# Optimization experiments

Measured on AMD Instinct MI355X. Metric: run time of the kernel, lower is better.

Reference implementation:

```python
import jax, jax.numpy as jnp
import numpy as np

B, N = 16, 4096
D_IN, D_OUT, HID, E = 128, 128, 256, 8
SG_HID = 16  # SharedGate hidden fixed at 16 in __init__


def setup_inputs() -> dict:
    key = jax.random.key(0)
    ks = jax.random.split(key, 6)
    s = 0.05
    return {
        "x": jax.random.normal(ks[0], (B, N, D_IN), dtype=jnp.float32),
        "active_experts": jnp.ones((B, E), dtype=jnp.int32),
        # SharedGate: fc1 [16, D_IN], fc2 [D_IN, 16] (torch Linear weight is [out, in])
        "sg_w1": jax.random.normal(ks[1], (SG_HID, D_IN), dtype=jnp.float32) * s,
        "sg_w2": jax.random.normal(ks[2], (D_IN, SG_HID), dtype=jnp.float32) * s,
        # TaskSpecificGate: E linears [1, D_IN] -> stacked [E, D_IN]
        "gate_w": jax.random.normal(ks[3], (E, D_IN), dtype=jnp.float32) * s,
        # Expert MLPs (no bias): fc1 [E, HID, D_IN], fc2 [E, D_OUT, HID]
        "exp_w1": jax.random.normal(ks[4], (E, HID, D_IN), dtype=jnp.float32) * s,
        "exp_w2": jax.random.normal(ks[5], (E, D_OUT, HID), dtype=jnp.float32) * s,
    }


def reference(x, active_experts, sg_w1, sg_w2, gate_w, exp_w1, exp_w2):
    b, n, d_in = x.shape
    xf = x.reshape(-1, d_in)  # [T, D_IN], T = B*N (node-level routing)

    # SharedGate with residual: fc2(relu(fc1(x))) + x
    shared = jnp.maximum(xf @ sg_w1.T, 0.0) @ sg_w2.T + xf  # [T, D_IN]

    # Task-specific gate: per-expert scalar scores, masked softmax over experts
    scores = (shared @ gate_w.T).reshape(b, n, -1)  # [B, N, E]
    mask = active_experts.astype(bool)[:, None, :]  # [B, 1, E]
    masked = jnp.where(mask, scores, -jnp.inf)
    weights = jax.nn.softmax(masked, axis=-1)  # [B, N, E]

    # All experts (dense): batched two-layer MLP per expert
    h = jnp.maximum(jnp.einsum("td,ehd->teh", xf, exp_w1), 0.0)  # [T, E, HID]
    out = jnp.einsum("teh,eoh->teo", h, exp_w2)  # [T, E, D_OUT]
    out_r = out.reshape(b, n, weights.shape[-1], -1)  # [B, N, E, D_OUT]

    # Gate-weighted combine over experts
    output_end = jnp.sum(out_r * weights[..., None], axis=2)  # [B, N, D_OUT]
    aux_loss = jnp.float32(0.0)  # sign=False
    return output_end, aux_loss
```

## Files before the change

### kernel.cpp

```cpp
#include <hip/hip_runtime.h>
#include <hip/hip_bf16.h>


typedef float f32x4 __attribute__((ext_vector_type(4)));
typedef short bf16x8 __attribute__((ext_vector_type(8)));

static __device__ __forceinline__ short f2bs(float f) {
  union { __hip_bfloat16 b; short s; } u;
  u.b = __float2bfloat16(f);
  return u.s;
}


__global__ void prep_kernel(const float* __restrict__ sg_w1,
                            const float* __restrict__ sg_w2,
                            const float* __restrict__ gate_w,
                            const float* __restrict__ exp_w1,
                            const float* __restrict__ exp_w2,
                            short* __restrict__ ws_s) {
  int idx = blockIdx.x * 256 + threadIdx.x;
  if (idx < 262144) {
    int e = idx >> 15, rem = idx & 32767;
    int frag = rem >> 9, lane = (rem >> 3) & 63, j = rem & 7;
    int hid = (frag >> 2) * 16 + (lane & 15);
    int k   = (frag & 3) * 32 + (lane >> 4) * 8 + j;
    ws_s[idx] = f2bs(exp_w1[(e * 256 + hid) * 128 + k]);
  } else if (idx < 524288) {
    int i2 = idx - 262144;
    int e = i2 >> 15, rem = i2 & 32767;
    int frag = rem >> 9, lane = (rem >> 3) & 63, j = rem & 7;
    int lg = lane >> 4, l15 = lane & 15;
    int o  = (frag >> 3) * 16 + l15;
    int ks = frag & 7;
    int h  = ks * 32 + (j < 4 ? lg * 4 + j : 16 + lg * 4 + (j - 4));
    ws_s[idx] = f2bs(exp_w2[(e * 128 + o) * 256 + h]);
  } else if (idx < 526336) {
    int i3 = idx - 524288;
    int k = i3 >> 9, lane = (i3 >> 3) & 63, j = i3 & 7;
    int lg = lane >> 4, l15 = lane & 15;
    ws_s[idx] = f2bs(sg_w1[l15 * 128 + k * 32 + lg * 8 + j]);
  } else if (idx < 528384) {
    int i4 = idx - 526336;
    int k = i4 >> 9, lane = (i4 >> 3) & 63, j = i4 & 7;
    int lg = lane >> 4, l15 = lane & 15;
    ws_s[idx] = (l15 < 8) ? f2bs(gate_w[l15 * 128 + k * 32 + lg * 8 + j]) : (short)0;
  } else if (idx < 528896) {
    int i5 = idx - 528384;
    int lane = (i5 >> 3) & 63, j = i5 & 7;
    int lg = lane >> 4, l15 = lane & 15;
    int kk = lg * 8 + j;
    if (l15 < 8 && kk < 16) {
      float acc = 0.f;
      for (int d = 0; d < 128; ++d) acc += gate_w[l15 * 128 + d] * sg_w2[d * 16 + kk];
      ws_s[idx] = f2bs(acc);
    } else {
      ws_s[idx] = 0;
    }
  }
}

__global__ __launch_bounds__(256, 1) void moe_kernel(
    const float* __restrict__ x, const int* __restrict__ active,
    const short* __restrict__ ws_s, float* __restrict__ out) {
  __shared__ short Ul[4][2560];

  const short* W1p  = ws_s;
  const short* W2p  = ws_s + 262144;
  const short* sg1p = ws_s + 524288;
  const short* gwp  = ws_s + 526336;
  const short* gcp  = ws_s + 528384;

  const int tid  = threadIdx.x;
  const int lane = tid & 63;
  const int wid  = tid >> 6;
  const int l15  = lane & 15;
  const int lg   = lane >> 4;
  const int tokw = blockIdx.x * 256 + wid * 64;

  short* Ulw = &Ul[wid][0];
  for (int i = lane; i < 1280; i += 64) ((int*)Ulw)[i] = 0;
  __syncthreads();

  bf16x8 xf[4][4];
  {
    int trow = tokw + l15;
#pragma unroll
    for (int m = 0; m < 4; ++m) {
      const float* xr = x + (size_t)(trow + m * 16) * 128;
#pragma unroll
      for (int k = 0; k < 4; ++k) {
        int c = k * 32 + lg * 8;
        float4 a = *(const float4*)(xr + c);
        float4 b = *(const float4*)(xr + c + 4);
        bf16x8 v;
        v[0] = f2bs(a.x); v[1] = f2bs(a.y); v[2] = f2bs(a.z); v[3] = f2bs(a.w);
        v[4] = f2bs(b.x); v[5] = f2bs(b.y); v[6] = f2bs(b.z); v[7] = f2bs(b.w);
        xf[m][k] = v;
      }
    }
  }

  f32x4 wreg[4];
  {
    bf16x8 sgf[4], gwf[4];
#pragma unroll
    for (int k = 0; k < 4; ++k) {
      sgf[k] = *(const bf16x8*)(sg1p + k * 512 + lane * 8);
      gwf[k] = *(const bf16x8*)(gwp  + k * 512 + lane * 8);
    }
#pragma unroll
    for (int m = 0; m < 4; ++m) {
      f32x4 acc = {0.f, 0.f, 0.f, 0.f};
#pragma unroll
      for (int k = 0; k < 4; ++k)
        acc = __builtin_amdgcn_mfma_f32_16x16x32_bf16(xf[m][k], sgf[k], acc, 0, 0, 0);
#pragma unroll
      for (int r = 0; r < 4; ++r)
        Ulw[(m * 16 + lg * 4 + r) * 40 + l15] = f2bs(fmaxf(acc[r], 0.f));
    }
    f32x4 sc[4];
#pragma unroll
    for (int m = 0; m < 4; ++m) {
      f32x4 acc = {0.f, 0.f, 0.f, 0.f};
#pragma unroll
      for (int k = 0; k < 4; ++k)
        acc = __builtin_amdgcn_mfma_f32_16x16x32_bf16(xf[m][k], gwf[k], acc, 0, 0, 0);
      sc[m] = acc;
    }
    __syncthreads();
    bf16x8 gcf = *(const bf16x8*)(gcp + lane * 8);
#pragma unroll
    for (int m = 0; m < 4; ++m) {
      bf16x8 uf = *(const bf16x8*)(Ulw + (m * 16 + l15) * 40 + lg * 8);
      sc[m] = __builtin_amdgcn_mfma_f32_16x16x32_bf16(uf, gcf, sc[m], 0, 0, 0);
    }
    int b = tokw >> 12;
    float am = (l15 < 8 && active[b * 8 + l15] != 0) ? 0.f : -3.0e38f;
#pragma unroll
    for (int m = 0; m < 4; ++m) {
      f32x4 w4;
#pragma unroll
      for (int r = 0; r < 4; ++r) {
        float s = sc[m][r] + am;
        float mx = s;
        mx = fmaxf(mx, __shfl_xor(mx, 1));
        mx = fmaxf(mx, __shfl_xor(mx, 2));
        mx = fmaxf(mx, __shfl_xor(mx, 4));
        float p = __expf(s - mx);
        float su = p;
        su += __shfl_xor(su, 1);
        su += __shfl_xor(su, 2);
        su += __shfl_xor(su, 4);
        w4[r] = p / su;
      }
      wreg[m] = w4;
    }
  }

  f32x4 acc2[4][8];
#pragma unroll
  for (int m = 0; m < 4; ++m)
#pragma unroll
    for (int o = 0; o < 8; ++o)
      acc2[m][o] = {0.f, 0.f, 0.f, 0.f};

  for (int e = 0; e < 8; ++e) {
    float wv[4];
    {
      int srcb = ((l15 >> 2) << 4) | e;
      int rp = l15 & 3;
#pragma unroll
      for (int m = 0; m < 4; ++m) {
        float q0 = __shfl(wreg[m][0], srcb), q1 = __shfl(wreg[m][1], srcb);
        float q2 = __shfl(wreg[m][2], srcb), q3 = __shfl(wreg[m][3], srcb);
        float lo = (rp & 1) ? q1 : q0, hi = (rp & 1) ? q3 : q2;
        wv[m] = (rp & 2) ? hi : lo;
      }
    }
    const short* w1e = W1p + e * 32768 + lane * 8;
    const short* w2e = W2p + e * 32768 + lane * 8;

    bf16x8 A1a[8], B2a[8], A1b[8], B2b[8];

    auto loadc = [&](bf16x8 (&A)[8], bf16x8 (&B)[8], int ks) {
#pragma unroll
      for (int i = 0; i < 8; ++i) {
        A[i] = *(const bf16x8*)(w1e + (ks * 8 + i) * 512);
        B[i] = *(const bf16x8*)(w2e + (i * 8 + ks) * 512);
      }
    };
    auto computec = [&](const bf16x8 (&A)[8], const bf16x8 (&B)[8]) {
      f32x4 a1[4][2];
#pragma unroll
      for (int m = 0; m < 4; ++m)
#pragma unroll
        for (int n = 0; n < 2; ++n) {
          f32x4 acc = {0.f, 0.f, 0.f, 0.f};
#pragma unroll
          for (int kx = 0; kx < 4; ++kx)
            acc = __builtin_amdgcn_mfma_f32_16x16x32_bf16(A[n * 4 + kx], xf[m][kx], acc, 0, 0, 0);
          a1[m][n] = acc;
        }
      bf16x8 hB[4];
#pragma unroll
      for (int m = 0; m < 4; ++m) {
        bf16x8 h;
#pragma unroll
        for (int r = 0; r < 4; ++r) {
          h[r]     = f2bs(fmaxf(a1[m][0][r], 0.f) * wv[m]);
          h[r + 4] = f2bs(fmaxf(a1[m][1][r], 0.f) * wv[m]);
        }
        hB[m] = h;
      }
#pragma unroll
      for (int o = 0; o < 8; ++o)
#pragma unroll
        for (int m = 0; m < 4; ++m)
          acc2[m][o] = __builtin_amdgcn_mfma_f32_16x16x32_bf16(B[o], hB[m], acc2[m][o], 0, 0, 0);
    };

    loadc(A1a, B2a, 0);
#pragma unroll
    for (int kk = 0; kk < 4; ++kk) {
      loadc(A1b, B2b, 2 * kk + 1);
      computec(A1a, B2a);
      if (kk < 3) loadc(A1a, B2a, 2 * kk + 2);
      computec(A1b, B2b);
    }
  }

#pragma unroll
  for (int m = 0; m < 4; ++m)
#pragma unroll
    for (int o = 0; o < 8; ++o)
      *(f32x4*)(out + (size_t)(tokw + m * 16 + l15) * 128 + o * 16 + lg * 4) = acc2[m][o];

  if (blockIdx.x == 0 && tid == 0) out[8388608] = 0.0f;
}

extern "C" void kernel_launch(void* const* d_in, const int* in_sizes, int n_in,
                              void* d_out, int out_size, void* d_ws, size_t ws_size,
                              hipStream_t stream) {
  const float* x      = (const float*)d_in[0];
  const int*   act    = (const int*)d_in[1];
  const float* sg_w1  = (const float*)d_in[2];
  const float* sg_w2  = (const float*)d_in[3];
  const float* gate_w = (const float*)d_in[4];
  const float* exp_w1 = (const float*)d_in[5];
  const float* exp_w2 = (const float*)d_in[6];
  short* ws_s = (short*)d_ws;
  float* out = (float*)d_out;

  prep_kernel<<<2066, 256, 0, stream>>>(sg_w1, sg_w2, gate_w, exp_w1, exp_w2, ws_s);
  moe_kernel<<<256, 256, 0, stream>>>(x, act, ws_s, out);
}
```

Before: 82.66 us.

## Split experts across two wave halves with LDS-staged async weight ring

Doubles the block to 512 threads. Each half of the waves handles four of the eight experts for the same 256 tokens, and the two halves' partial outputs are reduced through LDS in the epilogue. Expert weights are streamed into a triple-buffered LDS ring with global_load_lds, using explicit vmcnt waits and barriers, so all waves share one copy instead of each wave loading its own into registers. The intent is to raise the number of waves in flight and cut redundant weight traffic. The cost is heavier LDS use, a block barrier on every k-step, and an extra reduction pass.

```diff
diff --git a/kernel.cpp b/kernel.cpp
--- a/kernel.cpp
+++ b/kernel.cpp
@@ -9,6 +9,12 @@
   union { __hip_bfloat16 b; short s; } u;
   u.b = __float2bfloat16(f);
   return u.s;
+}
+
+static __device__ __forceinline__ unsigned pk2(float lo, float hi) {
+  union { __hip_bfloat162 b; unsigned u; } t;
+  t.b = __float22bfloat162_rn(make_float2(lo, hi));
+  return t.u;
 }
 
 
@@ -30,8 +36,9 @@
     int e = i2 >> 15, rem = i2 & 32767;
     int frag = rem >> 9, lane = (rem >> 3) & 63, j = rem & 7;
     int lg = lane >> 4, l15 = lane & 15;
-    int o  = (frag >> 3) * 16 + l15;
-    int ks = frag & 7;
+    int ks = frag >> 3;
+    int oi = frag & 7;
+    int o  = oi * 16 + l15;
     int h  = ks * 32 + (j < 4 ? lg * 4 + j : 16 + lg * 4 + (j - 4));
     ws_s[idx] = f2bs(exp_w2[(e * 128 + o) * 256 + h]);
   } else if (idx < 526336) {
@@ -59,10 +66,11 @@
   }
 }
 
-__global__ __launch_bounds__(256, 1) void moe_kernel(
+__global__ __launch_bounds__(512, 2) void moe_kernel(
     const float* __restrict__ x, const int* __restrict__ active,
     const short* __restrict__ ws_s, float* __restrict__ out) {
-  __shared__ short Ul[4][2560];
+  __shared__ __align__(16) short ringS[3 * 16384];
+  __shared__ short Ul[8][2560];
 
   const short* W1p  = ws_s;
   const short* W2p  = ws_s + 262144;
@@ -75,11 +83,32 @@
   const int wid  = tid >> 6;
   const int l15  = lane & 15;
   const int lg   = lane >> 4;
-  const int tokw = blockIdx.x * 256 + wid * 64;
+  const int lw   = wid & 3;
+  const int hf   = wid >> 2;
+  const int eb   = hf * 4;
+  const int tokw = blockIdx.x * 256 + lw * 64;
+
+  auto stage = [&](int q) {
+    int cq = (eb + (q >> 3)) * 8 + (q & 7);
+    short* db = &ringS[(q % 3) * 16384 + hf * 8192];
+#pragma unroll
+    for (int t = 0; t < 4; ++t) {
+      int f = lw * 4 + t;
+      const short* s = (f < 8)
+          ? (W1p + ((size_t)cq * 8 + f) * 512 + lane * 8)
+          : (W2p + ((size_t)cq * 8 + (f - 8)) * 512 + lane * 8);
+      __builtin_amdgcn_global_load_lds(
+          (const __attribute__((address_space(1))) void*)s,
+          (__attribute__((address_space(3))) void*)(&db[f * 512]),
+          16, 0, 0);
+    }
+  };
+
+  stage(0);
+  stage(1);
 
   short* Ulw = &Ul[wid][0];
   for (int i = lane; i < 1280; i += 64) ((int*)Ulw)[i] = 0;
-  __syncthreads();
 
   bf16x8 xf[4][4];
   {
@@ -99,9 +128,11 @@
       }
     }
   }
-
-  f32x4 wreg[4];
+  __syncthreads();
+
+  float wv4[4][4];
   {
+    f32x4 wreg[4];
     bf16x8 sgf[4], gwf[4];
 #pragma unroll
     for (int k = 0; k < 4; ++k) {
@@ -155,86 +186,100 @@
       }
       wreg[m] = w4;
     }
-  }
-
-  f32x4 acc2[4][8];
-#pragma unroll
-  for (int m = 0; m < 4; ++m)
-#pragma unroll
-    for (int o = 0; o < 8; ++o)
-      acc2[m][o] = {0.f, 0.f, 0.f, 0.f};
-
-  for (int e = 0; e < 8; ++e) {
-    float wv[4];
-    {
-      int srcb = ((l15 >> 2) << 4) | e;
+#pragma unroll
+    for (int e4 = 0; e4 < 4; ++e4) {
+      int srcb = ((l15 >> 2) << 4) | (eb + e4);
       int rp = l15 & 3;
 #pragma unroll
       for (int m = 0; m < 4; ++m) {
         float q0 = __shfl(wreg[m][0], srcb), q1 = __shfl(wreg[m][1], srcb);
         float q2 = __shfl(wreg[m][2], srcb), q3 = __shfl(wreg[m][3], srcb);
         float lo = (rp & 1) ? q1 : q0, hi = (rp & 1) ? q3 : q2;
-        wv[m] = (rp & 2) ? hi : lo;
-      }
-    }
-    const short* w1e = W1p + e * 32768 + lane * 8;
-    const short* w2e = W2p + e * 32768 + lane * 8;
-
-    bf16x8 A1a[8], B2a[8], A1b[8], B2b[8];
-
-    auto loadc = [&](bf16x8 (&A)[8], bf16x8 (&B)[8], int ks) {
-#pragma unroll
-      for (int i = 0; i < 8; ++i) {
-        A[i] = *(const bf16x8*)(w1e + (ks * 8 + i) * 512);
-        B[i] = *(const bf16x8*)(w2e + (i * 8 + ks) * 512);
-      }
-    };
-    auto computec = [&](const bf16x8 (&A)[8], const bf16x8 (&B)[8]) {
-      f32x4 a1[4][2];
-#pragma unroll
-      for (int m = 0; m < 4; ++m)
-#pragma unroll
-        for (int n = 0; n < 2; ++n) {
-          f32x4 acc = {0.f, 0.f, 0.f, 0.f};
+        wv4[e4][m] = (rp & 2) ? hi : lo;
+      }
+    }
+  }
+
+  f32x4 acc2[4][8];
+#pragma unroll
+  for (int m = 0; m < 4; ++m)
+#pragma unroll
+    for (int o = 0; o < 8; ++o)
+      acc2[m][o] = {0.f, 0.f, 0.f, 0.f};
+
+#pragma unroll
+  for (int e4 = 0; e4 < 4; ++e4) {
+#pragma unroll 1
+    for (int ks = 0; ks < 8; ++ks) {
+      const int p = e4 * 8 + ks;
+      if (p == 31) asm volatile("s_waitcnt vmcnt(0)" ::: "memory");
+      else         asm volatile("s_waitcnt vmcnt(4)" ::: "memory");
+      __builtin_amdgcn_sched_barrier(0);
+      __builtin_amdgcn_s_barrier();
+      __builtin_amdgcn_sched_barrier(0);
+      if (p + 2 < 32) stage(p + 2);
+
+      const short* rb = &ringS[(p % 3) * 16384 + hf * 8192];
+      __builtin_amdgcn_s_setprio(1);
+
+      union HU { unsigned u[4]; bf16x8 v; };
+      HU hu[4];
+#pragma unroll
+      for (int n = 0; n < 2; ++n) {
+        bf16x8 Af[4];
+#pragma unroll
+        for (int kx = 0; kx < 4; ++kx)
+          Af[kx] = *(const bf16x8*)(rb + (n * 4 + kx) * 512 + lane * 8);
+#pragma unroll
+        for (int m = 0; m < 4; ++m) {
+          f32x4 a = {0.f, 0.f, 0.f, 0.f};
 #pragma unroll
           for (int kx = 0; kx < 4; ++kx)
-            acc = __builtin_amdgcn_mfma_f32_16x16x32_bf16(A[n * 4 + kx], xf[m][kx], acc, 0, 0, 0);
-          a1[m][n] = acc;
+            a = __builtin_amdgcn_mfma_f32_16x16x32_bf16(Af[kx], xf[m][kx], a, 0, 0, 0);
+          float s = wv4[e4][m];
+          hu[m].u[n * 2]     = pk2(fmaxf(a[0], 0.f) * s, fmaxf(a[1], 0.f) * s);
+          hu[m].u[n * 2 + 1] = pk2(fmaxf(a[2], 0.f) * s, fmaxf(a[3], 0.f) * s);
         }
-      bf16x8 hB[4];
-#pragma unroll
-      for (int m = 0; m < 4; ++m) {
-        bf16x8 h;
-#pragma unroll
-        for (int r = 0; r < 4; ++r) {
-          h[r]     = f2bs(fmaxf(a1[m][0][r], 0.f) * wv[m]);
-          h[r + 4] = f2bs(fmaxf(a1[m][1][r], 0.f) * wv[m]);
+      }
+#pragma unroll
+      for (int o = 0; o < 8; ++o) {
+        bf16x8 Bf = *(const bf16x8*)(rb + 4096 + o * 512 + lane * 8);
+#pragma unroll
+        for (int m = 0; m < 4; ++m)
+          acc2[m][o] = __builtin_amdgcn_mfma_f32_16x16x32_bf16(Bf, hu[m].v, acc2[m][o], 0, 0, 0);
+      }
+      __builtin_amdgcn_s_setprio(0);
+    }
+  }
+
+  __syncthreads();
+  float* ep = (float*)ringS;
+#pragma unroll
+  for (int rr = 0; rr < 2; ++rr) {
+    if (hf == 1) {
+#pragma unroll
+      for (int mm = 0; mm < 2; ++mm) {
+#pragma unroll
+        for (int o = 0; o < 8; ++o)
+          *(f32x4*)&ep[(lw * 2 + mm) * 2112 + l15 * 132 + o * 16 + lg * 4] =
+              acc2[rr * 2 + mm][o];
+      }
+    }
+    __syncthreads();
+    if (hf == 0) {
+#pragma unroll
+      for (int mm = 0; mm < 2; ++mm) {
+#pragma unroll
+        for (int o = 0; o < 8; ++o) {
+          f32x4 v = *(const f32x4*)&ep[(lw * 2 + mm) * 2112 + l15 * 132 + o * 16 + lg * 4];
+          f32x4 r = acc2[rr * 2 + mm][o];
+          r[0] += v[0]; r[1] += v[1]; r[2] += v[2]; r[3] += v[3];
+          *(f32x4*)(out + (size_t)(tokw + (rr * 2 + mm) * 16 + l15) * 128 + o * 16 + lg * 4) = r;
         }
-        hB[m] = h;
-      }
-#pragma unroll
-      for (int o = 0; o < 8; ++o)
-#pragma unroll
-        for (int m = 0; m < 4; ++m)
-          acc2[m][o] = __builtin_amdgcn_mfma_f32_16x16x32_bf16(B[o], hB[m], acc2[m][o], 0, 0, 0);
-    };
-
-    loadc(A1a, B2a, 0);
-#pragma unroll
-    for (int kk = 0; kk < 4; ++kk) {
-      loadc(A1b, B2b, 2 * kk + 1);
-      computec(A1a, B2a);
-      if (kk < 3) loadc(A1a, B2a, 2 * kk + 2);
-      computec(A1b, B2b);
-    }
-  }
-
-#pragma unroll
-  for (int m = 0; m < 4; ++m)
-#pragma unroll
-    for (int o = 0; o < 8; ++o)
-      *(f32x4*)(out + (size_t)(tokw + m * 16 + l15) * 128 + o * 16 + lg * 4) = acc2[m][o];
-
+      }
+    }
+    __syncthreads();
+  }
   if (blockIdx.x == 0 && tid == 0) out[8388608] = 0.0f;
 }
 
@@ -252,5 +297,5 @@
   float* out = (float*)d_out;
 
   prep_kernel<<<2066, 256, 0, stream>>>(sg_w1, sg_w2, gate_w, exp_w1, exp_w2, ws_s);
-  moe_kernel<<<256, 256, 0, stream>>>(x, act, ws_s, out);
-}
+  moe_kernel<<<256, 512, 0, stream>>>(x, act, ws_s, out);
+}
```

Measured after the change: 107.5 us. +30.1%, slower.

## Split expert MLP across wave pairs and stage hidden activations in swizzled LDS

Applied to the files above, without the earlier changes.

The block grows to 512 threads, and each pair of waves shares a 64-token tile, each wave handling half the hidden and output columns. The gated first-layer activations go to an XOR-swizzled shared-memory buffer instead of being kept in registers. The second layer reads them back as MFMA fragments, and the W2 prepack layout changes to match. This halves per-wave accumulators and weight loads and raises occupancy, at the cost of LDS traffic, two barriers per expert, and losing the explicit double-buffered weight prefetch.

```diff
diff --git a/kernel.cpp b/kernel.cpp
--- a/kernel.cpp
+++ b/kernel.cpp
@@ -9,6 +9,12 @@
   union { __hip_bfloat16 b; short s; } u;
   u.b = __float2bfloat16(f);
   return u.s;
+}
+
+static __device__ __forceinline__ unsigned pk2(float lo, float hi) {
+  union { __hip_bfloat162 b; unsigned u; } t;
+  t.b = __float22bfloat162_rn(make_float2(lo, hi));
+  return t.u;
 }
 
 
@@ -30,9 +36,10 @@
     int e = i2 >> 15, rem = i2 & 32767;
     int frag = rem >> 9, lane = (rem >> 3) & 63, j = rem & 7;
     int lg = lane >> 4, l15 = lane & 15;
-    int o  = (frag >> 3) * 16 + l15;
+    int ot = frag >> 3;
     int ks = frag & 7;
-    int h  = ks * 32 + (j < 4 ? lg * 4 + j : 16 + lg * 4 + (j - 4));
+    int o  = ot * 16 + l15;
+    int h  = ks * 32 + lg * 8 + j;
     ws_s[idx] = f2bs(exp_w2[(e * 128 + o) * 256 + h]);
   } else if (idx < 526336) {
     int i3 = idx - 524288;
@@ -59,10 +66,10 @@
   }
 }
 
-__global__ __launch_bounds__(256, 1) void moe_kernel(
+__global__ __launch_bounds__(512) void moe_kernel(
     const float* __restrict__ x, const int* __restrict__ active,
     const short* __restrict__ ws_s, float* __restrict__ out) {
-  __shared__ short Ul[4][2560];
+  __shared__ __align__(16) short Hs[65536];
 
   const short* W1p  = ws_s;
   const short* W2p  = ws_s + 262144;
@@ -75,11 +82,14 @@
   const int wid  = tid >> 6;
   const int l15  = lane & 15;
   const int lg   = lane >> 4;
-  const int tokw = blockIdx.x * 256 + wid * 64;
-
-  short* Ulw = &Ul[wid][0];
+  const int wn   = wid & 1;
+  const int wm   = wid >> 1;
+  const int tokw = blockIdx.x * 256 + wm * 64;
+
+  char* Hw = (char*)(Hs + wm * 16384);
+
+  short* Ulw = Hs + wid * 2560;
   for (int i = lane; i < 1280; i += 64) ((int*)Ulw)[i] = 0;
-  __syncthreads();
 
   bf16x8 xf[4][4];
   {
@@ -99,6 +109,7 @@
       }
     }
   }
+  __syncthreads();
 
   f32x4 wreg[4];
   {
@@ -156,12 +167,13 @@
       wreg[m] = w4;
     }
   }
-
-  f32x4 acc2[4][8];
+  __syncthreads();
+
+  f32x4 acc2[4][4];
 #pragma unroll
   for (int m = 0; m < 4; ++m)
 #pragma unroll
-    for (int o = 0; o < 8; ++o)
+    for (int o = 0; o < 4; ++o)
       acc2[m][o] = {0.f, 0.f, 0.f, 0.f};
 
   for (int e = 0; e < 8; ++e) {
@@ -177,63 +189,60 @@
         wv[m] = (rp & 2) ? hi : lo;
       }
     }
+
     const short* w1e = W1p + e * 32768 + lane * 8;
+#pragma unroll
+    for (int n = 0; n < 8; ++n) {
+      int ht = wn * 8 + n;
+      bf16x8 Wf[4];
+#pragma unroll
+      for (int kx = 0; kx < 4; ++kx)
+        Wf[kx] = *(const bf16x8*)(w1e + (ht * 4 + kx) * 512);
+#pragma unroll
+      for (int m = 0; m < 4; ++m) {
+        f32x4 a = {0.f, 0.f, 0.f, 0.f};
+#pragma unroll
+        for (int kx = 0; kx < 4; ++kx)
+          a = __builtin_amdgcn_mfma_f32_16x16x32_bf16(Wf[kx], xf[m][kx], a, 0, 0, 0);
+        float s = wv[m];
+        uint2 w;
+        w.x = pk2(fmaxf(a[0], 0.f) * s, fmaxf(a[1], 0.f) * s);
+        w.y = pk2(fmaxf(a[2], 0.f) * s, fmaxf(a[3], 0.f) * s);
+        int row = m * 16 + l15;
+        int col = wn * 256 + n * 32 + lg * 8;
+        *(uint2*)(Hw + row * 512 + (col ^ ((row & 7) << 4))) = w;
+      }
+    }
+    __syncthreads();
+
     const short* w2e = W2p + e * 32768 + lane * 8;
-
-    bf16x8 A1a[8], B2a[8], A1b[8], B2b[8];
-
-    auto loadc = [&](bf16x8 (&A)[8], bf16x8 (&B)[8], int ks) {
-#pragma unroll
-      for (int i = 0; i < 8; ++i) {
-        A[i] = *(const bf16x8*)(w1e + (ks * 8 + i) * 512);
-        B[i] = *(const bf16x8*)(w2e + (i * 8 + ks) * 512);
-      }
-    };
-    auto computec = [&](const bf16x8 (&A)[8], const bf16x8 (&B)[8]) {
-      f32x4 a1[4][2];
-#pragma unroll
-      for (int m = 0; m < 4; ++m)
-#pragma unroll
-        for (int n = 0; n < 2; ++n) {
-          f32x4 acc = {0.f, 0.f, 0.f, 0.f};
-#pragma unroll
-          for (int kx = 0; kx < 4; ++kx)
-            acc = __builtin_amdgcn_mfma_f32_16x16x32_bf16(A[n * 4 + kx], xf[m][kx], acc, 0, 0, 0);
-          a1[m][n] = acc;
-        }
-      bf16x8 hB[4];
+#pragma unroll
+    for (int ks = 0; ks < 8; ++ks) {
+      bf16x8 hf[4];
 #pragma unroll
       for (int m = 0; m < 4; ++m) {
-        bf16x8 h;
-#pragma unroll
-        for (int r = 0; r < 4; ++r) {
-          h[r]     = f2bs(fmaxf(a1[m][0][r], 0.f) * wv[m]);
-          h[r + 4] = f2bs(fmaxf(a1[m][1][r], 0.f) * wv[m]);
-        }
-        hB[m] = h;
-      }
-#pragma unroll
-      for (int o = 0; o < 8; ++o)
+        int row = m * 16 + l15;
+        int col = ks * 64 + lg * 16;
+        hf[m] = *(const bf16x8*)(Hw + row * 512 + (col ^ ((row & 7) << 4)));
+      }
+#pragma unroll
+      for (int o = 0; o < 4; ++o) {
+        int ot = wn * 4 + o;
+        bf16x8 Bf = *(const bf16x8*)(w2e + (ot * 8 + ks) * 512);
 #pragma unroll
         for (int m = 0; m < 4; ++m)
-          acc2[m][o] = __builtin_amdgcn_mfma_f32_16x16x32_bf16(B[o], hB[m], acc2[m][o], 0, 0, 0);
-    };
-
-    loadc(A1a, B2a, 0);
-#pragma unroll
-    for (int kk = 0; kk < 4; ++kk) {
-      loadc(A1b, B2b, 2 * kk + 1);
-      computec(A1a, B2a);
-      if (kk < 3) loadc(A1a, B2a, 2 * kk + 2);
-      computec(A1b, B2b);
-    }
+          acc2[m][o] = __builtin_amdgcn_mfma_f32_16x16x32_bf16(Bf, hf[m], acc2[m][o], 0, 0, 0);
+      }
+    }
+    __syncthreads();
   }
 
 #pragma unroll
   for (int m = 0; m < 4; ++m)
 #pragma unroll
-    for (int o = 0; o < 8; ++o)
-      *(f32x4*)(out + (size_t)(tokw + m * 16 + l15) * 128 + o * 16 + lg * 4) = acc2[m][o];
+    for (int o = 0; o < 4; ++o)
+      *(f32x4*)(out + (size_t)(tokw + m * 16 + l15) * 128 + wn * 64 + o * 16 + lg * 4) =
+          acc2[m][o];
 
   if (blockIdx.x == 0 && tid == 0) out[8388608] = 0.0f;
 }
@@ -252,5 +261,5 @@
   float* out = (float*)d_out;
 
   prep_kernel<<<2066, 256, 0, stream>>>(sg_w1, sg_w2, gate_w, exp_w1, exp_w2, ws_s);
-  moe_kernel<<<256, 256, 0, stream>>>(x, act, ws_s, out);
-}
+  moe_kernel<<<256, 512, 0, stream>>>(x, act, ws_s, out);
+}
```

Result: slower. 132.7 us (+60.5%).
